# Optimization experiments

Measured on AMD Instinct MI355X. Metric: run time of the kernel, lower is better.

## Reference

```python
import jax, jax.numpy as jnp
import numpy as np

N = 65536        # batch (nodes)
IN_SIZE = 256    # irreps1.dim * irreps2.dim = 16*16
OUT_SIZE = 256
NNZ = 2048       # nonzero Clebsch-Gordan entries


def setup_inputs() -> dict:
    key = jax.random.key(0)
    k1, k2, k3, k4 = jax.random.split(key, 4)
    inp = jax.random.normal(k1, (N, IN_SIZE), dtype=jnp.float32)
    scale = jax.random.normal(k2, (NNZ,), dtype=jnp.float32)
    M_in = jax.random.randint(k3, (NNZ,), 0, IN_SIZE, dtype=jnp.int64)
    M = jnp.sort(jax.random.randint(k4, (NNZ,), 0, OUT_SIZE, dtype=jnp.int64))
    return {"input": inp, "scale": scale, "M_in": M_in, "M": M, "out_size": OUT_SIZE}


def reference(input, scale, M_in, M, out_size):
    # sparse_scale: out[n, M[k]] += scale[k] * input[n, M_in[k]]
    gathered = input[:, M_in] * scale  # [N, nnz]
    # segment-sum over the nnz axis into out_size output slots (M is sorted)
    out = jax.ops.segment_sum(gathered.T, M, num_segments=out_size,
                              indices_are_sorted=True).T  # [N, out_size]
    return out
```

## Files before the change

kernel.cpp:

```cpp
#include <hip/hip_runtime.h>
#include <hip/hip_bf16.h>

#define IN_SZ   256
#define OUT_SZ  256
#define NNZ_C   2048
#define NB      16
#define BM      64
#define KFULL   256

typedef __attribute__((ext_vector_type(8))) short bf16x8;
typedef __attribute__((ext_vector_type(4))) float f32x4;

static __device__ __forceinline__ short f2bf(float f) {
    __hip_bfloat16 h = __float2bfloat16(f);
    return (short)__builtin_bit_cast(unsigned short, h);
}


__global__ void build_w(const float* __restrict__ scale,
                        const int*   __restrict__ M_in,
                        const int*   __restrict__ M,
                        unsigned short* __restrict__ wb)
{
    __shared__ float row[IN_SZ];
    const int j = blockIdx.x;
    const int t = threadIdx.x;

#pragma unroll
    for (int i = t; i < IN_SZ; i += 64) row[i] = 0.f;

    int lo = 0, hi = NNZ_C;
    while (lo < hi) { int mid = (lo + hi) >> 1; if (M[mid] < j)     lo  = mid + 1; else hi  = mid; }
    int lo2 = lo, hi2 = NNZ_C;
    while (lo2 < hi2) { int mid = (lo2 + hi2) >> 1; if (M[mid] < j + 1) lo2 = mid + 1; else hi2 = mid; }

    __syncthreads();
    for (int k = lo + t; k < lo2; k += 64)
        atomicAdd(&row[M_in[k]], scale[k]);
    __syncthreads();

    const int wn = j >> 6, n = (j >> 4) & 3, l15 = j & 15;
#pragma unroll
    for (int kk = t; kk < IN_SZ; kk += 64) {
        int kt = kk >> 6, kf = (kk >> 5) & 1, lhi = (kk >> 3) & 3, e = kk & 7;
        int lane = lhi * 16 + l15;
        int c = (((wn * 4 + n) * 4 + kt) * 2 + kf) * 64 + lane;
        wb[c * 8 + e] = (unsigned short)f2bf(row[kk]);
    }
}


__global__ __launch_bounds__(256, 2)
void gemm_fullk(const float* __restrict__ input,
                const bf16x8* __restrict__ wfrag,
                float* __restrict__ out)
{
    __shared__ float sA[BM * KFULL];

    const int tid  = threadIdx.x;
    const int lane = tid & 63;
    const int w    = tid >> 6;
    const int l15  = lane & 15, lhi = lane >> 4;
    const long row0 = (long)blockIdx.x * BM;

#pragma unroll
    for (int it = 0; it < 16; ++it) {
        const int r = w * 16 + it;
        const float* src = input + (row0 + r) * IN_SZ + ((lane ^ (r & 7)) << 2);
        __builtin_amdgcn_global_load_lds(
            (const __attribute__((address_space(1))) unsigned int*)src,
            (__attribute__((address_space(3))) unsigned int*)&sA[r * KFULL],
            16, 0, 0);
    }

    f32x4 acc[4][4];
#pragma unroll
    for (int m = 0; m < 4; ++m)
#pragma unroll
        for (int n = 0; n < 4; ++n)
            acc[m][n] = (f32x4){0.f, 0.f, 0.f, 0.f};

    bf16x8 Breg[2][8];
#pragma unroll
    for (int i = 0; i < 8; ++i)
        Breg[0][i] = wfrag[(((w * 4 + (i >> 1)) * 4 + 0) * 2 + (i & 1)) * 64 + lane];

    __syncthreads();

#pragma unroll
    for (int kt = 0; kt < 4; ++kt) {
        const int cur = kt & 1;
        if (kt < 3) {
#pragma unroll
            for (int i = 0; i < 8; ++i)
                Breg[cur ^ 1][i] =
                    wfrag[(((w * 4 + (i >> 1)) * 4 + (kt + 1)) * 2 + (i & 1)) * 64 + lane];
        }
#pragma unroll
        for (int kf = 0; kf < 2; ++kf) {
#pragma unroll
            for (int m = 0; m < 4; ++m) {
                const int r  = m * 16 + l15;
                const int g0 = kt * 16 + kf * 8 + lhi * 2;
                f32x4 a0 = *(const f32x4*)&sA[r * KFULL + ((g0 ^ (r & 7)) << 2)];
                f32x4 a1 = *(const f32x4*)&sA[r * KFULL + (((g0 + 1) ^ (r & 7)) << 2)];
                bf16x8 u;
                u[0] = f2bf(a0[0]); u[1] = f2bf(a0[1]);
                u[2] = f2bf(a0[2]); u[3] = f2bf(a0[3]);
                u[4] = f2bf(a1[0]); u[5] = f2bf(a1[1]);
                u[6] = f2bf(a1[2]); u[7] = f2bf(a1[3]);
#pragma unroll
                for (int n = 0; n < 4; ++n)
                    acc[m][n] = __builtin_amdgcn_mfma_f32_16x16x32_bf16(
                        u, Breg[cur][n * 2 + kf], acc[m][n], 0, 0, 0);
            }
        }
    }

#pragma unroll
    for (int m = 0; m < 4; ++m) {
        long r0 = row0 + m * 16 + lhi * 4;
#pragma unroll
        for (int n = 0; n < 4; ++n) {
            int col = w * 64 + n * 16 + l15;
#pragma unroll
            for (int r = 0; r < 4; ++r)
                out[(r0 + r) * OUT_SZ + col] = acc[m][n][r];
        }
    }
}


__global__ __launch_bounds__(256, 4)
void sparse_tp_kernel(const float* __restrict__ input,
                      const float* __restrict__ scale,
                      const int*   __restrict__ M_in,
                      const int*   __restrict__ M,
                      float*       __restrict__ out,
                      int N)
{
    __shared__ float s_in[NB * IN_SZ];
    __shared__ float s_scale[NNZ_C];
    __shared__ int   s_min[NNZ_C];
    __shared__ int   s_seg[OUT_SZ + 1];

    const int tid  = threadIdx.x;
    const int base = blockIdx.x * NB;

    {
        const float4* sc4  = reinterpret_cast<const float4*>(scale);
        const int4*   mi4  = reinterpret_cast<const int4*>(M_in);
        float4*       ssc4 = reinterpret_cast<float4*>(s_scale);
        int4*         smi4 = reinterpret_cast<int4*>(s_min);
        for (int v = tid; v < NNZ_C / 4; v += 256) { ssc4[v] = sc4[v]; smi4[v] = mi4[v]; }
    }
    {
        const float4* in4 = reinterpret_cast<const float4*>(input + (size_t)base * IN_SZ);
        float4*       si4 = reinterpret_cast<float4*>(s_in);
        for (int v = tid; v < NB * IN_SZ / 4; v += 256) {
            int row = v / (IN_SZ / 4);
            if (base + row < N) si4[v] = in4[v];
        }
    }
    {
        int j = tid, lo = 0, hi = NNZ_C;
        while (lo < hi) { int mid = (lo + hi) >> 1; if (M[mid] < j) lo = mid + 1; else hi = mid; }
        s_seg[j] = lo;
        if (tid == 0) s_seg[OUT_SZ] = NNZ_C;
    }
    __syncthreads();

    float acc[NB];
#pragma unroll
    for (int i = 0; i < NB; ++i) acc[i] = 0.f;

    const int j = tid;
    const int k1 = s_seg[j + 1];
    for (int k = s_seg[j]; k < k1; ++k) {
        const float s = s_scale[k];
        const int   m = s_min[k];
#pragma unroll
        for (int i = 0; i < NB; ++i) acc[i] += s * s_in[i * IN_SZ + m];
    }

    float* orow = out + (size_t)base * OUT_SZ + j;
#pragma unroll
    for (int i = 0; i < NB; ++i)
        if (base + i < N) orow[(size_t)i * OUT_SZ] = acc[i];
}


extern "C" void kernel_launch(void* const* d_in, const int* in_sizes, int n_in,
                              void* d_out, int out_size, void* d_ws, size_t ws_size,
                              hipStream_t stream)
{
    const float* input = (const float*)d_in[0];
    const float* scale = (const float*)d_in[1];
    const int*   M_in  = (const int*)d_in[2];
    const int*   M     = (const int*)d_in[3];
    float*       out   = (float*)d_out;

    const int N = in_sizes[0] / IN_SZ;

    if (ws_size >= (size_t)(128 * 1024) && (N % BM) == 0) {
        unsigned short* wb = (unsigned short*)d_ws;
        build_w   <<<OUT_SZ, 64, 0, stream>>>(scale, M_in, M, wb);
        gemm_fullk<<<N / BM, 256, 0, stream>>>(input, (const bf16x8*)wb, out);
    } else {
        sparse_tp_kernel<<<(N + NB - 1) / NB, 256, 0, stream>>>(input, scale, M_in, M, out, N);
    }
}
```

Baseline: 131.2 us.

## Double-buffer K-tiles of A in LDS with 128-row, 8-wave GEMM blocks

Replaces the full-K single-shot LDS load of a 64-row tile with a 128-row block of 8 waves (2x4 over M and N) that streams the fp32 input in 64-wide K slices through two LDS buffers. The next slice is staged with global_load_lds while MFMAs run on the current one. The goal is to overlap HBM loads with compute and to halve per-block B-fragment reloads per row. In exchange it adds a barrier per K step, and LDS per block shrinks, which changes occupancy.

```diff
diff --git a/kernel.cpp b/kernel.cpp
--- a/kernel.cpp
+++ b/kernel.cpp
@@ -5,8 +5,8 @@
 #define OUT_SZ  256
 #define NNZ_C   2048
 #define NB      16
-#define BM      64
-#define KFULL   256
+#define BM      128
+#define BK      64
 
 typedef __attribute__((ext_vector_type(8))) short bf16x8;
 typedef __attribute__((ext_vector_type(4))) float f32x4;
@@ -50,28 +50,34 @@
 }
 
 
-__global__ __launch_bounds__(256, 2)
-void gemm_fullk(const float* __restrict__ input,
+__global__ __launch_bounds__(512, 4)
+void gemm_bm128(const float* __restrict__ input,
                 const bf16x8* __restrict__ wfrag,
                 float* __restrict__ out)
 {
-    __shared__ float sA[BM * KFULL];
+    __shared__ float sA[2][BM * BK];
 
     const int tid  = threadIdx.x;
     const int lane = tid & 63;
-    const int w    = tid >> 6;
+    const int wid  = tid >> 6;
+    const int wm   = wid >> 2;
+    const int wn   = wid & 3;
     const int l15  = lane & 15, lhi = lane >> 4;
     const long row0 = (long)blockIdx.x * BM;
 
-#pragma unroll
-    for (int it = 0; it < 16; ++it) {
-        const int r = w * 16 + it;
-        const float* src = input + (row0 + r) * IN_SZ + ((lane ^ (r & 7)) << 2);
-        __builtin_amdgcn_global_load_lds(
-            (const __attribute__((address_space(1))) unsigned int*)src,
-            (__attribute__((address_space(3))) unsigned int*)&sA[r * KFULL],
-            16, 0, 0);
-    }
+    auto stage = [&](int buf, int kt) {
+#pragma unroll
+        for (int it = 0; it < 4; ++it) {
+            const int c = wid * 4 + it;
+            const int r = c * 4 + lhi;
+            const int g = l15 ^ (r & 7);
+            const float* src = input + (row0 + r) * IN_SZ + kt * BK + g * 4;
+            __builtin_amdgcn_global_load_lds(
+                (const __attribute__((address_space(1))) unsigned int*)src,
+                (__attribute__((address_space(3))) unsigned int*)&sA[buf][c * 256],
+                16, 0, 0);
+        }
+    };
 
     f32x4 acc[4][4];
 #pragma unroll
@@ -81,29 +87,32 @@
             acc[m][n] = (f32x4){0.f, 0.f, 0.f, 0.f};
 
     bf16x8 Breg[2][8];
+
+    stage(0, 0);
 #pragma unroll
     for (int i = 0; i < 8; ++i)
-        Breg[0][i] = wfrag[(((w * 4 + (i >> 1)) * 4 + 0) * 2 + (i & 1)) * 64 + lane];
-
+        Breg[0][i] = wfrag[(((wn * 4 + (i >> 1)) * 4 + 0) * 2 + (i & 1)) * 64 + lane];
     __syncthreads();
 
 #pragma unroll
     for (int kt = 0; kt < 4; ++kt) {
         const int cur = kt & 1;
         if (kt < 3) {
+            stage(cur ^ 1, kt + 1);
 #pragma unroll
             for (int i = 0; i < 8; ++i)
                 Breg[cur ^ 1][i] =
-                    wfrag[(((w * 4 + (i >> 1)) * 4 + (kt + 1)) * 2 + (i & 1)) * 64 + lane];
-        }
+                    wfrag[(((wn * 4 + (i >> 1)) * 4 + (kt + 1)) * 2 + (i & 1)) * 64 + lane];
+        }
+
 #pragma unroll
         for (int kf = 0; kf < 2; ++kf) {
 #pragma unroll
             for (int m = 0; m < 4; ++m) {
-                const int r  = m * 16 + l15;
-                const int g0 = kt * 16 + kf * 8 + lhi * 2;
-                f32x4 a0 = *(const f32x4*)&sA[r * KFULL + ((g0 ^ (r & 7)) << 2)];
-                f32x4 a1 = *(const f32x4*)&sA[r * KFULL + (((g0 + 1) ^ (r & 7)) << 2)];
+                const int r  = wm * 64 + m * 16 + l15;
+                const int g0 = kf * 8 + lhi * 2;
+                f32x4 a0 = *(const f32x4*)&sA[cur][r * BK + (((g0    ) ^ (r & 7)) << 2)];
+                f32x4 a1 = *(const f32x4*)&sA[cur][r * BK + (((g0 + 1) ^ (r & 7)) << 2)];
                 bf16x8 u;
                 u[0] = f2bf(a0[0]); u[1] = f2bf(a0[1]);
                 u[2] = f2bf(a0[2]); u[3] = f2bf(a0[3]);
@@ -115,14 +124,15 @@
                         u, Breg[cur][n * 2 + kf], acc[m][n], 0, 0, 0);
             }
         }
+        if (kt < 3) __syncthreads();
     }
 
 #pragma unroll
     for (int m = 0; m < 4; ++m) {
-        long r0 = row0 + m * 16 + lhi * 4;
+        long r0 = row0 + wm * 64 + m * 16 + lhi * 4;
 #pragma unroll
         for (int n = 0; n < 4; ++n) {
-            int col = w * 64 + n * 16 + l15;
+            int col = wn * 64 + n * 16 + l15;
 #pragma unroll
             for (int r = 0; r < 4; ++r)
                 out[(r0 + r) * OUT_SZ + col] = acc[m][n][r];
@@ -205,7 +215,7 @@
     if (ws_size >= (size_t)(128 * 1024) && (N % BM) == 0) {
         unsigned short* wb = (unsigned short*)d_ws;
         build_w   <<<OUT_SZ, 64, 0, stream>>>(scale, M_in, M, wb);
-        gemm_fullk<<<N / BM, 256, 0, stream>>>(input, (const bf16x8*)wb, out);
+        gemm_bm128<<<N / BM, 512, 0, stream>>>(input, (const bf16x8*)wb, out);
     } else {
         sparse_tp_kernel<<<(N + NB - 1) / NB, 256, 0, stream>>>(input, scale, M_in, M, out, N);
     }
```

Measured after the change: 131.0 us. Within noise of the previous version (-0.2%).
